# Optimization experiments

Hardware: AMD Instinct MI355X
Metric: run time of the kernel (lower is better)

Reference implementation:

```python
import jax, jax.numpy as jnp
import numpy as np
import itertools

DIM = 384
KEY_DIM = 32
NUM_HEADS = 8
ATTN_RATIO = 4
RESOLUTION = 7
D = ATTN_RATIO * KEY_DIM          # 128
DH = D * NUM_HEADS                # 1024
H_QKV = DH + 2 * KEY_DIM * NUM_HEADS  # 1536
B = 2048
N = RESOLUTION ** 2               # 49


def _build_bias_idxs():
    points = list(itertools.product(range(RESOLUTION), range(RESOLUTION)))
    attention_offsets = {}
    idxs = []
    for p1 in points:
        for p2 in points:
            offset = (abs(p1[0] - p2[0]), abs(p1[1] - p2[1]))
            if offset not in attention_offsets:
                attention_offsets[offset] = len(attention_offsets)
            idxs.append(attention_offsets[offset])
    return np.array(idxs, dtype=np.int32).reshape(N, N), len(attention_offsets)


def setup_inputs() -> dict:
    key = jax.random.key(0)
    ks = jax.random.split(key, 6)
    bias_idxs_np, n_offsets = _build_bias_idxs()  # n_offsets == 49 for resolution 7
    x = jax.random.normal(ks[0], (B, N, DIM), dtype=jnp.float32)
    qkv_w = jax.random.normal(ks[1], (H_QKV, DIM), dtype=jnp.float32) * (DIM ** -0.5)
    qkv_b = jnp.zeros((H_QKV,), dtype=jnp.float32)
    proj_w = jax.random.normal(ks[2], (DIM, DH), dtype=jnp.float32) * (DH ** -0.5)
    proj_b = jnp.zeros((DIM,), dtype=jnp.float32)
    attn_bias = jax.random.normal(ks[3], (NUM_HEADS, n_offsets), dtype=jnp.float32) * 0.02
    bias_idxs = jnp.asarray(bias_idxs_np)
    return {"x": x, "qkv_w": qkv_w, "qkv_b": qkv_b, "proj_w": proj_w,
            "proj_b": proj_b, "attn_bias": attn_bias, "bias_idxs": bias_idxs}


def reference(x, qkv_w, qkv_b, proj_w, proj_b, attn_bias, bias_idxs):
    Bb, Nn, _ = x.shape
    scale = KEY_DIM ** -0.5
    qkv = x @ qkv_w.T + qkv_b                       # [B, N, 1536]
    qkv = qkv.reshape(Bb, Nn, NUM_HEADS, KEY_DIM + KEY_DIM + D)
    q = qkv[..., :KEY_DIM]                          # [B, N, H, kd]
    k = qkv[..., KEY_DIM:2 * KEY_DIM]               # [B, N, H, kd]
    v = qkv[..., 2 * KEY_DIM:]                      # [B, N, H, d]
    bias = attn_bias[:, bias_idxs]                  # [H, N, N] gathered rel-pos bias
    attn = jnp.einsum('bnhk,bmhk->bhnm', q, k) * scale + bias
    attn = jax.nn.softmax(attn, axis=-1)
    out = jnp.einsum('bhnm,bmhd->bnhd', attn, v).reshape(Bb, Nn, DH)
    return out @ proj_w.T + proj_b                  # [B, N, dim]
```

## Files before the change

kernel.cpp:

```cpp
#include <hip/hip_runtime.h>
#include <cstddef>
#include <cstdint>

#define TOK    49
#define KD     32
#define NH     8
#define DHEAD  128
#define HQKV   1536
#define DHTOT  1024
#define DIMM   384

typedef unsigned short u16;
typedef float  f32x4  __attribute__((ext_vector_type(4)));
typedef __bf16 bf16x8 __attribute__((ext_vector_type(8)));

typedef const __attribute__((address_space(1))) void gas_void;
typedef __attribute__((address_space(3))) void las_void;

static __device__ __forceinline__ u16 f2bf(float f) {
    unsigned int u = __builtin_bit_cast(unsigned int, f);
    return (u16)((u + 0x7fffu + ((u >> 16) & 1u)) >> 16);
}

static __device__ __forceinline__ int swz(int row, int c) {
    return (row << 6) + ((((c >> 3) ^ (row & 7)) << 3) | (c & 7));
}

static __device__ __forceinline__ int swzV(int row, int c) {
    return (row << 6) + ((((c >> 3) ^ (row & 7) ^ ((row >> 3) & 7)) << 3) | (c & 7));
}

static __device__ __forceinline__ int xcd_chunk(int bid, int nwg) {
    const int xcd = bid & 7, slot = bid >> 3;
    const int q = nwg >> 3, r = nwg & 7;
    return (xcd < r ? xcd * (q + 1) : r * (q + 1) + (xcd - r) * q) + slot;
}

#define BAR() __builtin_amdgcn_s_barrier()
#define WAIT_VM6() asm volatile("s_waitcnt vmcnt(6)" ::: "memory")
#define WAIT_VM0() asm volatile("s_waitcnt vmcnt(0)" ::: "memory")
#define LGKM0_BAR() do { asm volatile("s_waitcnt lgkmcnt(0)" ::: "memory"); \
                         __builtin_amdgcn_s_barrier(); } while (0)

__global__ __launch_bounds__(256)
void cast_swz(const float* __restrict__ in, u16* __restrict__ out, int K8, long nchunk)
{
    long i = (long)blockIdx.x * 256 + threadIdx.x;
    const long stride = (long)gridDim.x * 256;
    for (; i < nchunk; i += stride) {
        const long row = i / K8;
        const int  c8  = (int)(i - row * K8);
        const int  slot = c8 & 7, tpan = c8 >> 3;
        float4 v0 = reinterpret_cast<const float4*>(in)[i * 2];
        float4 v1 = reinterpret_cast<const float4*>(in)[i * 2 + 1];
        uint4 o;
        o.x = f2bf(v0.x) | ((unsigned)f2bf(v0.y) << 16);
        o.y = f2bf(v0.z) | ((unsigned)f2bf(v0.w) << 16);
        o.z = f2bf(v1.x) | ((unsigned)f2bf(v1.y) << 16);
        o.w = f2bf(v1.z) | ((unsigned)f2bf(v1.w) << 16);
        *reinterpret_cast<uint4*>(out + row * (long)K8 * 8 + tpan * 64 +
                                  ((slot ^ ((int)row & 7)) << 3)) = o;
    }
}

__global__ __launch_bounds__(256)
void bias_expand(const float* __restrict__ attn_bias, const int* __restrict__ idxs,
                 float* __restrict__ bias_full, int n_off)
{
    int i = blockIdx.x * 256 + threadIdx.x;
    if (i < NH * TOK * TOK) {
        int h = i / (TOK * TOK), s = i - h * (TOK * TOK);
        bias_full[i] = attn_bias[h * n_off + idxs[s]];
    }
}

static __device__ __forceinline__ int frag_off(int row, int ks8fg) {
    return (row << 6) + (((ks8fg ^ (row & 7)) << 3));
}

__global__ __launch_bounds__(256)
void gemm_qkv(const u16* __restrict__ A,
              const u16* __restrict__ W,
              const float* __restrict__ bias,
              u16* __restrict__ qkvb, int M)
{
    const int K = DIMM;
    const int NB = HQKV / 128;
    const int nwg = (M / 64) * NB;
    const int wgid = xcd_chunk(blockIdx.x, nwg);
    const int bm = (wgid / NB) * 64;
    const int bn = (wgid % NB) * 128;

    __shared__ u16 Alds[2][64 * 64];
    __shared__ u16 Blds[2][128 * 64];

    const int t    = threadIdx.x;
    const int lane = t & 63;
    const int wv   = t >> 6;
    const int lrow = lane >> 3;
    const int lcol = (lane & 7) * 8;
    const int frow = lane & 15;
    const int fg   = lane >> 4;

    f32x4 acc[4][2];
    #pragma unroll
    for (int mi = 0; mi < 4; ++mi)
        #pragma unroll
        for (int nc = 0; nc < 2; ++nc) acc[mi][nc] = (f32x4)0.0f;

    auto STAGE = [&](int buf, int k0) {
        #pragma unroll
        for (int i = 0; i < 2; ++i) {
            const int c   = i * 4 + wv;
            const int row = c * 8 + lrow;
            __builtin_amdgcn_global_load_lds((gas_void*)(A + (size_t)(bm + row) * K + k0 + lcol),
                                             (las_void*)(&Alds[buf][c * 512]), 16, 0, 0);
        }
        #pragma unroll
        for (int i = 0; i < 4; ++i) {
            const int c   = i * 4 + wv;
            const int row = c * 8 + lrow;
            __builtin_amdgcn_global_load_lds((gas_void*)(W + (size_t)(bn + row) * K + k0 + lcol),
                                             (las_void*)(&Blds[buf][c * 512]), 16, 0, 0);
        }
    };

    STAGE(0, 0);
    STAGE(1, 64);

    const int NT = 6;
    for (int ts = 0; ts < NT; ++ts) {
        if (ts < NT - 1) { WAIT_VM6(); }
        else             { WAIT_VM0(); }
        BAR();
        const u16* Ab = Alds[ts & 1];
        const u16* Bb = Blds[ts & 1];
        #pragma unroll
        for (int ks = 0; ks < 2; ++ks) {
            const int sl = ks * 4 + fg;
            bf16x8 af[4], bf[2];
            #pragma unroll
            for (int mi = 0; mi < 4; ++mi)
                af[mi] = *reinterpret_cast<const bf16x8*>(&Ab[frag_off(mi * 16 + frow, sl)]);
            #pragma unroll
            for (int nc = 0; nc < 2; ++nc)
                bf[nc] = *reinterpret_cast<const bf16x8*>(&Bb[frag_off(wv * 32 + nc * 16 + frow, sl)]);
            #pragma unroll
            for (int mi = 0; mi < 4; ++mi)
                #pragma unroll
                for (int nc = 0; nc < 2; ++nc)
                    acc[mi][nc] = __builtin_amdgcn_mfma_f32_16x16x32_bf16(af[mi], bf[nc], acc[mi][nc], 0, 0, 0);
        }
        BAR();
        if (ts < NT - 2) STAGE(ts & 1, (ts + 2) * 64);
    }

    const int rbase = (lane >> 4) * 4;
    #pragma unroll
    for (int nc = 0; nc < 2; ++nc) {
        const int col = bn + wv * 32 + nc * 16 + frow;
        const float bv = bias[col];
        #pragma unroll
        for (int mi = 0; mi < 4; ++mi) {
            #pragma unroll
            for (int j = 0; j < 4; ++j) {
                const int row = bm + mi * 16 + rbase + j;
                qkvb[(size_t)row * HQKV + col] = f2bf(acc[mi][nc][j] + bv);
            }
        }
    }
}

__global__ __launch_bounds__(256)
void gemm_bf16_nt(const u16* __restrict__ A, const u16* __restrict__ W,
                  const float* __restrict__ bias, float* __restrict__ C,
                  int M, int N, int K)
{
    const int NB = N / 128;
    const int nwg = (M / 64) * NB;
    const int wgid = xcd_chunk(blockIdx.x, nwg);
    const int bm = (wgid / NB) * 64;
    const int bn = (wgid % NB) * 128;

    __shared__ u16 Alds[2][64 * 64];
    __shared__ u16 Blds[2][128 * 64];

    const int t    = threadIdx.x;
    const int lane = t & 63;
    const int wv   = t >> 6;
    const int lrow = lane >> 3;
    const int lcol = (lane & 7) * 8;
    const int frow = lane & 15;
    const int fg   = lane >> 4;

    f32x4 acc[4][2];
    #pragma unroll
    for (int mi = 0; mi < 4; ++mi)
        #pragma unroll
        for (int nc = 0; nc < 2; ++nc) acc[mi][nc] = (f32x4)0.0f;

    auto STAGE = [&](int buf, int k0) {
        #pragma unroll
        for (int i = 0; i < 2; ++i) {
            const int c   = i * 4 + wv;
            const int row = c * 8 + lrow;
            __builtin_amdgcn_global_load_lds((gas_void*)(A + (size_t)(bm + row) * K + k0 + lcol),
                                             (las_void*)(&Alds[buf][c * 512]), 16, 0, 0);
        }
        #pragma unroll
        for (int i = 0; i < 4; ++i) {
            const int c   = i * 4 + wv;
            const int row = c * 8 + lrow;
            __builtin_amdgcn_global_load_lds((gas_void*)(W + (size_t)(bn + row) * K + k0 + lcol),
                                             (las_void*)(&Blds[buf][c * 512]), 16, 0, 0);
        }
    };

    const int NT = K / 64;
    STAGE(0, 0);
    STAGE(1, 64);

    for (int ts = 0; ts < NT; ++ts) {
        if (ts < NT - 1) { WAIT_VM6(); }
        else             { WAIT_VM0(); }
        BAR();
        const u16* Ab = Alds[ts & 1];
        const u16* Bb = Blds[ts & 1];
        #pragma unroll
        for (int ks = 0; ks < 2; ++ks) {
            const int sl = ks * 4 + fg;
            bf16x8 af[4], bf[2];
            #pragma unroll
            for (int mi = 0; mi < 4; ++mi)
                af[mi] = *reinterpret_cast<const bf16x8*>(&Ab[frag_off(mi * 16 + frow, sl)]);
            #pragma unroll
            for (int nc = 0; nc < 2; ++nc)
                bf[nc] = *reinterpret_cast<const bf16x8*>(&Bb[frag_off(wv * 32 + nc * 16 + frow, sl)]);
            #pragma unroll
            for (int mi = 0; mi < 4; ++mi)
                #pragma unroll
                for (int nc = 0; nc < 2; ++nc)
                    acc[mi][nc] = __builtin_amdgcn_mfma_f32_16x16x32_bf16(af[mi], bf[nc], acc[mi][nc], 0, 0, 0);
        }
        BAR();
        if (ts < NT - 2) STAGE(ts & 1, (ts + 2) * 64);
    }

    const int rbase = (lane >> 4) * 4;
    #pragma unroll
    for (int nc = 0; nc < 2; ++nc) {
        const int col = bn + wv * 32 + nc * 16 + frow;
        const float bv = bias[col];
        #pragma unroll
        for (int mi = 0; mi < 4; ++mi) {
            #pragma unroll
            for (int j = 0; j < 4; ++j) {
                const int row = bm + mi * 16 + rbase + j;
                C[(size_t)row * N + col] = acc[mi][nc][j] + bv;
            }
        }
    }
}

#define NCH 5
struct Regs { uint4 v[NCH]; };

static __device__ __forceinline__ void load_regs(Regs& r, const u16* __restrict__ base, int t)
{
    #pragma unroll
    for (int k = 0; k < NCH; ++k) {
        const int idx = t + k * 256;
        if (idx < TOK * 24) {
            const int n = idx / 24, c = idx - n * 24;
            r.v[k] = *reinterpret_cast<const uint4*>(base + (size_t)n * HQKV + c * 8);
        }
    }
}

static __device__ __forceinline__ void write_lds(const Regs& r, u16* __restrict__ QK,
                                                 u16* __restrict__ V, int t)
{
    #pragma unroll
    for (int k = 0; k < NCH; ++k) {
        const int idx = t + k * 256;
        if (idx < TOK * 24) {
            const int n = idx / 24, c24 = idx - n * 24;
            if (c24 < 8) {
                *reinterpret_cast<uint4*>(&QK[(n << 6) + ((c24 ^ (n & 7)) << 3)]) = r.v[k];
            } else {
                const int d0 = (c24 - 8) * 8;
                u16 vals[8];
                *reinterpret_cast<uint4*>(vals) = r.v[k];
                #pragma unroll
                for (int e = 0; e < 8; ++e)
                    V[swzV(d0 + e, n)] = vals[e];
            }
        }
    }
}

static __device__ __forceinline__ void attn_head(
    const u16* __restrict__ QK, const u16* __restrict__ V,
    float* __restrict__ S, u16* __restrict__ Ps,
    const float* __restrict__ bh_bias, u16* __restrict__ ab,
    int b, int h, int t)
{
    const int lane = t & 63;
    const int w    = t >> 6;
    const int fr   = lane & 15;
    const int fg   = lane >> 4;

    bf16x8 qf = *reinterpret_cast<const bf16x8*>(&QK[swz(16 * w + fr, fg * 8)]);
    f32x4 sacc[4];
    #pragma unroll
    for (int nj = 0; nj < 4; ++nj) {
        bf16x8 kf = *reinterpret_cast<const bf16x8*>(&QK[swz(16 * nj + fr, 32 + fg * 8)]);
        sacc[nj] = __builtin_amdgcn_mfma_f32_16x16x32_bf16(qf, kf, (f32x4)0.0f, 0, 0, 0);
    }

    const float scale = 0.17677669529663687f;
    #pragma unroll
    for (int nj = 0; nj < 4; ++nj) {
        #pragma unroll
        for (int j = 0; j < 4; ++j) {
            const int row = 16 * w + fg * 4 + j;
            const int col = 16 * nj + fr;
            const int rn = row < TOK ? row : TOK - 1;
            const int cm = col < TOK ? col : TOK - 1;
            S[row * 80 + col] = sacc[nj][j] * scale + bh_bias[rn * TOK + cm];
        }
    }
    LGKM0_BAR();

    {
        const int n = t >> 2, j = t & 3;
        const float* Sr = &S[n * 80];
        float v[16];
        #pragma unroll
        for (int e = 0; e < 8; ++e) v[e]     = Sr[8 * j + e];
        #pragma unroll
        for (int e = 0; e < 8; ++e) v[8 + e] = Sr[32 + 8 * j + e];

        float mx = -1e30f;
        #pragma unroll
        for (int e = 0; e < 8; ++e) mx = fmaxf(mx, v[e]);
        #pragma unroll
        for (int e = 0; e < 8; ++e)
            if (32 + 8 * j + e < TOK) mx = fmaxf(mx, v[8 + e]);
        mx = fmaxf(mx, __shfl_xor(mx, 1, 4));
        mx = fmaxf(mx, __shfl_xor(mx, 2, 4));

        float sum = 0.f;
        #pragma unroll
        for (int e = 0; e < 8; ++e) { v[e] = __expf(v[e] - mx); sum += v[e]; }
        #pragma unroll
        for (int e = 0; e < 8; ++e) {
            const float ev = (32 + 8 * j + e < TOK) ? __expf(v[8 + e] - mx) : 0.f;
            v[8 + e] = ev; sum += ev;
        }
        sum += __shfl_xor(sum, 1, 4);
        sum += __shfl_xor(sum, 2, 4);
        const float inv = 1.f / sum;

        uint4 o;
        o.x = f2bf(v[0] * inv)  | ((unsigned)f2bf(v[1] * inv)  << 16);
        o.y = f2bf(v[2] * inv)  | ((unsigned)f2bf(v[3] * inv)  << 16);
        o.z = f2bf(v[4] * inv)  | ((unsigned)f2bf(v[5] * inv)  << 16);
        o.w = f2bf(v[6] * inv)  | ((unsigned)f2bf(v[7] * inv)  << 16);
        *reinterpret_cast<uint4*>(&Ps[swz(n, 8 * j)]) = o;
        o.x = f2bf(v[8] * inv)  | ((unsigned)f2bf(v[9] * inv)  << 16);
        o.y = f2bf(v[10] * inv) | ((unsigned)f2bf(v[11] * inv) << 16);
        o.z = f2bf(v[12] * inv) | ((unsigned)f2bf(v[13] * inv) << 16);
        o.w = f2bf(v[14] * inv) | ((unsigned)f2bf(v[15] * inv) << 16);
        *reinterpret_cast<uint4*>(&Ps[swz(n, 32 + 8 * j)]) = o;
    }
    LGKM0_BAR();

    f32x4 oacc[8];
    #pragma unroll
    for (int nj = 0; nj < 8; ++nj) oacc[nj] = (f32x4)0.0f;
    #pragma unroll
    for (int ks = 0; ks < 2; ++ks) {
        bf16x8 pf = *reinterpret_cast<const bf16x8*>(&Ps[swz(16 * w + fr, ks * 32 + fg * 8)]);
        #pragma unroll
        for (int nj = 0; nj < 8; ++nj) {
            bf16x8 vf = *reinterpret_cast<const bf16x8*>(&V[swzV(16 * nj + fr, ks * 32 + fg * 8)]);
            oacc[nj] = __builtin_amdgcn_mfma_f32_16x16x32_bf16(pf, vf, oacc[nj], 0, 0, 0);
        }
    }

    #pragma unroll
    for (int nj = 0; nj < 8; ++nj) {
        const int d = 16 * nj + fr;
        const int c = h * DHEAD + d;
        const int tp = c >> 6, sl = (c >> 3) & 7, cc = c & 7;
        #pragma unroll
        for (int j = 0; j < 4; ++j) {
            const int n = 16 * w + fg * 4 + j;
            if (n < TOK) {
                const int gr = b * TOK + n;
                ab[(size_t)gr * DHTOT + (tp << 6) + (((sl ^ (gr & 7)) << 3) | cc)] = f2bf(oacc[nj][j]);
            }
        }
    }
}

__global__ __launch_bounds__(256)
void attn_mfma(const u16* __restrict__ qkvb,
               const float* __restrict__ bias_full,
               u16* __restrict__ ab)
{
    __shared__ __align__(16) u16  QKs[64 * 64];
    __shared__ __align__(16) u16  Vts[128 * 64];
    __shared__ __align__(16) float S[64 * 80];
    __shared__ __align__(16) u16  Ps[64 * 64];

    const int t  = threadIdx.x;
    const int b  = blockIdx.x;
    const int h0 = blockIdx.y * 4;
    const u16* base = qkvb + (size_t)b * TOK * HQKV;

    if (t < 128 * 2) {
        const int row = t >> 1, sl = 6 + (t & 1);
        *reinterpret_cast<uint4*>(&Vts[(row << 6) +
            (((sl ^ (row & 7) ^ ((row >> 3) & 7)) & 7) << 3)]) = make_uint4(0, 0, 0, 0);
    }
    __syncthreads();

    const u16* qrow = base + h0 * 192;
    for (int flat = t; flat < TOK * 24; flat += 256) {
        const int n = flat / 24, c24 = flat - n * 24;
        uint4 u = *reinterpret_cast<const uint4*>(qrow + (size_t)n * HQKV + c24 * 8);
        if (c24 < 8) {
            *reinterpret_cast<uint4*>(&QKs[(n << 6) + ((c24 ^ (n & 7)) << 3)]) = u;
        } else {
            const int d0 = (c24 - 8) * 8;
            u16 vals[8];
            *reinterpret_cast<uint4*>(vals) = u;
            #pragma unroll
            for (int e = 0; e < 8; ++e)
                Vts[swzV(d0 + e, n)] = vals[e];
        }
    }

    Regs r;
    #pragma unroll
    for (int i = 0; i < 4; ++i) {
        if (i > 0) write_lds(r, QKs, Vts, t);
        if (i < 3) load_regs(r, base + (h0 + i + 1) * 192, t);
        LGKM0_BAR();
        attn_head(QKs, Vts, S, Ps, bias_full + (h0 + i) * (TOK * TOK), ab, b, h0 + i, t);
        LGKM0_BAR();
    }
}

extern "C" void kernel_launch(void* const* d_in, const int* in_sizes, int n_in,
                              void* d_out, int out_size, void* d_ws, size_t ws_size,
                              hipStream_t stream)
{
    const float* x         = (const float*)d_in[0];
    const float* qkv_w     = (const float*)d_in[1];
    const float* qkv_b     = (const float*)d_in[2];
    const float* proj_w    = (const float*)d_in[3];
    const float* proj_b    = (const float*)d_in[4];
    const float* attn_bias = (const float*)d_in[5];
    const int*   bias_idxs = (const int*)d_in[6];

    const int Mtot  = in_sizes[0] / DIMM;
    const int Btot  = Mtot / TOK;
    const int n_off = in_sizes[5] / NH;

    const size_t nWq = (size_t)HQKV * DIMM;
    const size_t nWp = (size_t)DIMM * DHTOT;
    float* bias_full = (float*)d_ws;
    u16*   wq        = (u16*)((char*)d_ws + 76832);
    u16*   wp        = wq + nWq;
    u16*   dyn       = wp + nWp;
    const size_t fixed_bytes = 76832 + (nWq + nWp) * sizeof(u16);
    const size_t per_batch = (size_t)TOK * (DIMM + HQKV + DHTOT) * 2;

    if (ws_size <= fixed_bytes) return;
    long BcL = (long)((ws_size - fixed_bytes) / per_batch);
    int Bc = (int)((BcL / 128) * 128);
    if (Bc <= 0) return;
    if (Bc > Btot) Bc = Btot;

    cast_swz<<<dim3(288), 256, 0, stream>>>(qkv_w, wq, DIMM / 8, (long)HQKV * (DIMM / 8));
    cast_swz<<<dim3(192), 256, 0, stream>>>(proj_w, wp, DHTOT / 8, (long)DIMM * (DHTOT / 8));
    bias_expand<<<dim3((NH * TOK * TOK + 255) / 256), 256, 0, stream>>>(attn_bias, bias_idxs, bias_full, n_off);

    for (int b0 = 0; b0 < Btot; b0 += Bc) {
        const int bc = (b0 + Bc <= Btot) ? Bc : (Btot - b0);
        const int Mc = bc * TOK;

        u16* xb   = dyn;
        u16* qkvb = xb   + (size_t)Bc * TOK * DIMM;
        u16* abb  = qkvb + (size_t)Bc * TOK * HQKV;

        const float* xc   = x + (size_t)b0 * TOK * DIMM;
        float*       outc = (float*)d_out + (size_t)b0 * TOK * DIMM;

        cast_swz<<<dim3(2048), 256, 0, stream>>>(xc, xb, DIMM / 8, (long)Mc * (DIMM / 8));

        gemm_qkv<<<dim3((Mc / 64) * (HQKV / 128)), 256, 0, stream>>>(xb, wq, qkv_b, qkvb, Mc);

        attn_mfma<<<dim3(bc, NH / 4), 256, 0, stream>>>(qkvb, bias_full, abb);

        gemm_bf16_nt<<<dim3((Mc / 64) * (DIMM / 128)), 256, 0, stream>>>(abb, wp, proj_b, outc, Mc, DIMM, DHTOT);
    }
}
```

Baseline: 652.7 us.

## Widen QKV GEMM tile to 256 columns and run all heads per attention block

The QKV GEMM now computes a 64x256 output tile per workgroup using two B panels. Each A tile is reused across twice as many columns, and the grid is halved. The wait count is raised to match the extra in-flight loads. The attention kernel now processes all 8 heads in one block per batch instead of splitting heads across two blocks, with the head loop no longer unrolled. The trade-off is higher LDS and register use in the GEMM, and fewer, longer attention blocks with less parallelism.

```diff
diff --git a/kernel.cpp b/kernel.cpp
--- a/kernel.cpp
+++ b/kernel.cpp
@@ -37,8 +37,9 @@
 }
 
 #define BAR() __builtin_amdgcn_s_barrier()
-#define WAIT_VM6() asm volatile("s_waitcnt vmcnt(6)" ::: "memory")
-#define WAIT_VM0() asm volatile("s_waitcnt vmcnt(0)" ::: "memory")
+#define WAIT_VM6()  asm volatile("s_waitcnt vmcnt(6)"  ::: "memory")
+#define WAIT_VM10() asm volatile("s_waitcnt vmcnt(10)" ::: "memory")
+#define WAIT_VM0()  asm volatile("s_waitcnt vmcnt(0)"  ::: "memory")
 #define LGKM0_BAR() do { asm volatile("s_waitcnt lgkmcnt(0)" ::: "memory"); \
                          __builtin_amdgcn_s_barrier(); } while (0)
 
@@ -85,14 +86,15 @@
               u16* __restrict__ qkvb, int M)
 {
     const int K = DIMM;
-    const int NB = HQKV / 128;
-    const int nwg = (M / 64) * NB;
+    const int NB2 = HQKV / 256;
+    const int nwg = (M / 64) * NB2;
     const int wgid = xcd_chunk(blockIdx.x, nwg);
-    const int bm = (wgid / NB) * 64;
-    const int bn = (wgid % NB) * 128;
+    const int bm = (wgid / NB2) * 64;
+    const int bn = (wgid % NB2) * 256;
 
     __shared__ u16 Alds[2][64 * 64];
-    __shared__ u16 Blds[2][128 * 64];
+    __shared__ u16 B0lds[2][128 * 64];
+    __shared__ u16 B1lds[2][128 * 64];
 
     const int t    = threadIdx.x;
     const int lane = t & 63;
@@ -102,11 +104,11 @@
     const int frow = lane & 15;
     const int fg   = lane >> 4;
 
-    f32x4 acc[4][2];
+    f32x4 acc0[4][2], acc1[4][2];
     #pragma unroll
     for (int mi = 0; mi < 4; ++mi)
         #pragma unroll
-        for (int nc = 0; nc < 2; ++nc) acc[mi][nc] = (f32x4)0.0f;
+        for (int nc = 0; nc < 2; ++nc) { acc0[mi][nc] = (f32x4)0.0f; acc1[mi][nc] = (f32x4)0.0f; }
 
     auto STAGE = [&](int buf, int k0) {
         #pragma unroll
@@ -121,7 +123,14 @@
             const int c   = i * 4 + wv;
             const int row = c * 8 + lrow;
             __builtin_amdgcn_global_load_lds((gas_void*)(W + (size_t)(bn + row) * K + k0 + lcol),
-                                             (las_void*)(&Blds[buf][c * 512]), 16, 0, 0);
+                                             (las_void*)(&B0lds[buf][c * 512]), 16, 0, 0);
+        }
+        #pragma unroll
+        for (int i = 0; i < 4; ++i) {
+            const int c   = i * 4 + wv;
+            const int row = c * 8 + lrow;
+            __builtin_amdgcn_global_load_lds((gas_void*)(W + (size_t)(bn + 128 + row) * K + k0 + lcol),
+                                             (las_void*)(&B1lds[buf][c * 512]), 16, 0, 0);
         }
     };
 
@@ -130,26 +139,31 @@
 
     const int NT = 6;
     for (int ts = 0; ts < NT; ++ts) {
-        if (ts < NT - 1) { WAIT_VM6(); }
+        if (ts < NT - 1) { WAIT_VM10(); }
         else             { WAIT_VM0(); }
         BAR();
-        const u16* Ab = Alds[ts & 1];
-        const u16* Bb = Blds[ts & 1];
+        const u16* Ab  = Alds[ts & 1];
+        const u16* B0b = B0lds[ts & 1];
+        const u16* B1b = B1lds[ts & 1];
         #pragma unroll
         for (int ks = 0; ks < 2; ++ks) {
             const int sl = ks * 4 + fg;
-            bf16x8 af[4], bf[2];
+            bf16x8 af[4], b0[2], b1[2];
             #pragma unroll
             for (int mi = 0; mi < 4; ++mi)
                 af[mi] = *reinterpret_cast<const bf16x8*>(&Ab[frag_off(mi * 16 + frow, sl)]);
             #pragma unroll
-            for (int nc = 0; nc < 2; ++nc)
-                bf[nc] = *reinterpret_cast<const bf16x8*>(&Bb[frag_off(wv * 32 + nc * 16 + frow, sl)]);
+            for (int nc = 0; nc < 2; ++nc) {
+                b0[nc] = *reinterpret_cast<const bf16x8*>(&B0b[frag_off(wv * 32 + nc * 16 + frow, sl)]);
+                b1[nc] = *reinterpret_cast<const bf16x8*>(&B1b[frag_off(wv * 32 + nc * 16 + frow, sl)]);
+            }
             #pragma unroll
             for (int mi = 0; mi < 4; ++mi)
                 #pragma unroll
-                for (int nc = 0; nc < 2; ++nc)
-                    acc[mi][nc] = __builtin_amdgcn_mfma_f32_16x16x32_bf16(af[mi], bf[nc], acc[mi][nc], 0, 0, 0);
+                for (int nc = 0; nc < 2; ++nc) {
+                    acc0[mi][nc] = __builtin_amdgcn_mfma_f32_16x16x32_bf16(af[mi], b0[nc], acc0[mi][nc], 0, 0, 0);
+                    acc1[mi][nc] = __builtin_amdgcn_mfma_f32_16x16x32_bf16(af[mi], b1[nc], acc1[mi][nc], 0, 0, 0);
+                }
         }
         BAR();
         if (ts < NT - 2) STAGE(ts & 1, (ts + 2) * 64);
@@ -157,15 +171,19 @@
 
     const int rbase = (lane >> 4) * 4;
     #pragma unroll
-    for (int nc = 0; nc < 2; ++nc) {
-        const int col = bn + wv * 32 + nc * 16 + frow;
-        const float bv = bias[col];
-        #pragma unroll
-        for (int mi = 0; mi < 4; ++mi) {
-            #pragma unroll
-            for (int j = 0; j < 4; ++j) {
-                const int row = bm + mi * 16 + rbase + j;
-                qkvb[(size_t)row * HQKV + col] = f2bf(acc[mi][nc][j] + bv);
+    for (int half = 0; half < 2; ++half) {
+        #pragma unroll
+        for (int nc = 0; nc < 2; ++nc) {
+            const int col = bn + half * 128 + wv * 32 + nc * 16 + frow;
+            const float bv = bias[col];
+            #pragma unroll
+            for (int mi = 0; mi < 4; ++mi) {
+                #pragma unroll
+                for (int j = 0; j < 4; ++j) {
+                    const int row = bm + mi * 16 + rbase + j;
+                    const float v = half ? acc1[mi][nc][j] : acc0[mi][nc][j];
+                    qkvb[(size_t)row * HQKV + col] = f2bf(v + bv);
+                }
             }
         }
     }
@@ -415,9 +433,8 @@
     __shared__ __align__(16) float S[64 * 80];
     __shared__ __align__(16) u16  Ps[64 * 64];
 
-    const int t  = threadIdx.x;
-    const int b  = blockIdx.x;
-    const int h0 = blockIdx.y * 4;
+    const int t = threadIdx.x;
+    const int b = blockIdx.x;
     const u16* base = qkvb + (size_t)b * TOK * HQKV;
 
     if (t < 128 * 2) {
@@ -427,10 +444,9 @@
     }
     __syncthreads();
 
-    const u16* qrow = base + h0 * 192;
     for (int flat = t; flat < TOK * 24; flat += 256) {
         const int n = flat / 24, c24 = flat - n * 24;
-        uint4 u = *reinterpret_cast<const uint4*>(qrow + (size_t)n * HQKV + c24 * 8);
+        uint4 u = *reinterpret_cast<const uint4*>(base + (size_t)n * HQKV + c24 * 8);
         if (c24 < 8) {
             *reinterpret_cast<uint4*>(&QKs[(n << 6) + ((c24 ^ (n & 7)) << 3)]) = u;
         } else {
@@ -444,12 +460,12 @@
     }
 
     Regs r;
-    #pragma unroll
-    for (int i = 0; i < 4; ++i) {
+    #pragma unroll 1
+    for (int i = 0; i < NH; ++i) {
         if (i > 0) write_lds(r, QKs, Vts, t);
-        if (i < 3) load_regs(r, base + (h0 + i + 1) * 192, t);
+        if (i < NH - 1) load_regs(r, base + (i + 1) * 192, t);
         LGKM0_BAR();
-        attn_head(QKs, Vts, S, Ps, bias_full + (h0 + i) * (TOK * TOK), ab, b, h0 + i, t);
+        attn_head(QKs, Vts, S, Ps, bias_full + i * (TOK * TOK), ab, b, i, t);
         LGKM0_BAR();
     }
 }
@@ -502,9 +518,9 @@
 
         cast_swz<<<dim3(2048), 256, 0, stream>>>(xc, xb, DIMM / 8, (long)Mc * (DIMM / 8));
 
-        gemm_qkv<<<dim3((Mc / 64) * (HQKV / 128)), 256, 0, stream>>>(xb, wq, qkv_b, qkvb, Mc);
-
-        attn_mfma<<<dim3(bc, NH / 4), 256, 0, stream>>>(qkvb, bias_full, abb);
+        gemm_qkv<<<dim3((Mc / 64) * (HQKV / 256)), 256, 0, stream>>>(xb, wq, qkv_b, qkvb, Mc);
+
+        attn_mfma<<<dim3(bc), 256, 0, stream>>>(qkvb, bias_full, abb);
 
         gemm_bf16_nt<<<dim3((Mc / 64) * (DIMM / 128)), 256, 0, stream>>>(abb, wp, proj_b, outc, Mc, DIMM, DHTOT);
     }
```

Result: faster. 624.2 us (-4.4%).
